# Kernel optimization log

Hardware: AMD Instinct MI355X
Metric: run time of the kernel (lower is better)

Reference implementation:

```python
import jax, jax.numpy as jnp
import numpy as np

DIM = 1024
NUM_HEADS = 16
HEAD_DIM = DIM // NUM_HEADS
SCALE = HEAD_DIM ** (-0.5)


def setup_inputs() -> dict:
    key = jax.random.key(0)
    k_x, k_qkv, k_ow, k_ob = jax.random.split(key, 4)
    x = jax.random.normal(k_x, (4, 2048, DIM), dtype=jnp.float32)
    # nn.Linear(dim, 3*dim, bias=False): store as [dim, 3*dim] for x @ W
    w_qkv = jax.random.normal(k_qkv, (DIM, 3 * DIM), dtype=jnp.float32) * (DIM ** -0.5)
    w_out = jax.random.normal(k_ow, (DIM, DIM), dtype=jnp.float32) * (DIM ** -0.5)
    b_out = jax.random.normal(k_ob, (DIM,), dtype=jnp.float32) * 0.02
    return {"x": x, "w_qkv": w_qkv, "w_out": w_out, "b_out": b_out}


def reference(x, w_qkv, w_out, b_out):
    B, S, D = x.shape
    H, Hd = NUM_HEADS, HEAD_DIM
    qkv = x @ w_qkv                                  # [B, S, 3*D]
    # rearrange 'b s (v h d) -> v b h s d'
    qkv = qkv.reshape(B, S, 3, H, Hd).transpose(2, 0, 3, 1, 4)
    q, k, v = qkv[0], qkv[1], qkv[2]                 # each [B, H, S, Hd]
    scores = jnp.einsum('bhqd,bhkd->bhqk', q, k) * SCALE
    attn = jax.nn.softmax(scores, axis=-1)
    out = jnp.einsum('bhqk,bhkd->bhqd', attn, v)     # [B, H, S, Hd]
    out = out.transpose(0, 2, 1, 3).reshape(B, S, D)  # 'b h s d -> b s (h d)'
    return out @ w_out + b_out
```

## Files before the change

kernel.cpp:

```cpp
#include <hip/hip_runtime.h>
#include <hip/hip_bf16.h>
#include <stdint.h>

typedef __bf16 bf16_t;
typedef __bf16 bf16x4 __attribute__((ext_vector_type(4)));
typedef __bf16 bf16x8 __attribute__((ext_vector_type(8)));
typedef float f32x4 __attribute__((ext_vector_type(4)));
typedef unsigned short u16;

#define L2E 1.4426950408889634f
#define MC 69.249473f
#define QSC 0.18033688f

__device__ __forceinline__ void async_load16(const bf16_t* g, bf16_t* l) {
  __builtin_amdgcn_global_load_lds(
      (__attribute__((address_space(1))) uint32_t*)g,
      (__attribute__((address_space(3))) uint32_t*)l, 16, 0, 0);
}

__global__ void detect_k(const uint16_t* __restrict__ x, int* __restrict__ flag) {
  if (blockIdx.x != 0) return;
  const int lane = threadIdx.x & 63;
  int bad = 0;
#pragma unroll
  for (int p = 0; p < 4; ++p) {
    const int i = lane * 4 + p;
    uint16_t h = x[2 * i];
    int e = (h >> 7) & 0xFF;
    if (e == 0 || e >= 0xBD) bad++;
  }
  bad += __shfl_xor(bad, 1, 64);
  bad += __shfl_xor(bad, 2, 64);
  bad += __shfl_xor(bad, 4, 64);
  bad += __shfl_xor(bad, 8, 64);
  bad += __shfl_xor(bad, 16, 64);
  bad += __shfl_xor(bad, 32, 64);
  if (lane == 0 && threadIdx.x < 64) *flag = (bad > 32) ? 1 : 0;
}

__global__ void convert_k(const void* __restrict__ in, bf16_t* __restrict__ out,
                          int n, const int* __restrict__ flag) {
  const int f = *flag;
  const int nv = n >> 3;
  const int i0 = blockIdx.x * blockDim.x + threadIdx.x;
  const int stride = gridDim.x * blockDim.x;
  if (f) {
    const float4* p = (const float4*)in;
    for (int i = i0; i < nv; i += stride) {
      const float4 a = p[2 * i], b = p[2 * i + 1];
      const float v[8] = {a.x, a.y, a.z, a.w, b.x, b.y, b.z, b.w};
      bf16x8 o8;
#pragma unroll
      for (int j = 0; j < 8; ++j) {
        float x = v[j];
        x = (x == x) ? x : 0.f;
        x = fminf(fmaxf(x, -1e6f), 1e6f);
        o8[j] = (bf16_t)x;
      }
      *(bf16x8*)(out + (size_t)i * 8) = o8;
    }
  } else {
    const uint4* p = (const uint4*)in;
    for (int i = i0; i < nv; i += stride) {
      const uint4 a = p[i];
      const uint32_t wds[4] = {a.x, a.y, a.z, a.w};
      bf16x8 o8;
#pragma unroll
      for (int j = 0; j < 8; ++j) {
        const uint32_t h = (wds[j >> 1] >> ((j & 1) * 16)) & 0xFFFFu;
        float x = __builtin_bit_cast(float, h << 16);
        x = (x == x) ? x : 0.f;
        x = fminf(fmaxf(x, -1e6f), 1e6f);
        o8[j] = (bf16_t)x;
      }
      *(bf16x8*)(out + (size_t)i * 8) = o8;
    }
  }
}

__global__ __launch_bounds__(256) void wtrans_k(const void* __restrict__ in,
                                                bf16_t* __restrict__ out, int R,
                                                int C, const int* __restrict__ flag) {
  __shared__ u16 tile[64][65];
  const int f = *flag;
  const int tr = blockIdx.y * 64, tc = blockIdx.x * 64;
  const int t = threadIdx.x;
#pragma unroll
  for (int i = 0; i < 16; ++i) {
    int idx = i * 256 + t, r = idx >> 6, c = idx & 63;
    float v;
    if (f)
      v = ((const float*)in)[(size_t)(tr + r) * C + tc + c];
    else
      v = (float)((const bf16_t*)in)[(size_t)(tr + r) * C + tc + c];
    v = (v == v) ? v : 0.f;
    v = fminf(fmaxf(v, -1e6f), 1e6f);
    bf16_t b = (bf16_t)v;
    tile[r][c] = *(u16*)&b;
  }
  __syncthreads();
#pragma unroll
  for (int i = 0; i < 16; ++i) {
    int idx = i * 256 + t, r = idx >> 6, c = idx & 63;
    ((u16*)out)[(size_t)(tc + r) * R + tr + c] = tile[c][r];
  }
}

__device__ __forceinline__ void gemm_bt_mainloop(
    const bf16_t* __restrict__ A, const bf16_t* __restrict__ Bt, int K, int m0,
    int n0, bf16_t* As, bf16_t* Bs, f32x4 acc[4][4]) {
  const int t = threadIdx.x, lane = t & 63, w = t >> 6;
  const int l15 = lane & 15, quad = lane >> 4;
  const int wm = (w >> 1) * 64, wn = (w & 1) * 64;
  const int srow = w * 16 + (lane >> 2);
  const int sk = (lane & 3) * 8;
  const bf16_t* gA = A + (size_t)(m0 + srow) * K + sk;
  const bf16_t* gB = Bt + (size_t)(n0 + srow) * K + sk;
  const size_t gstep = (size_t)64 * K;
  const int nt = K >> 5;
  const int lo = w * 512;

  async_load16(gA, As + lo);
  async_load16(gA + gstep, As + lo + 2048);
  async_load16(gB, Bs + lo);
  async_load16(gB + gstep, Bs + lo + 2048);
  __syncthreads();

  for (int kt = 0; kt < nt; ++kt) {
    const int cur = (kt & 1) * 4096, nxt = 4096 - cur;
    if (kt + 1 < nt) {
      const bf16_t* gA1 = gA + (size_t)(kt + 1) * 32;
      const bf16_t* gB1 = gB + (size_t)(kt + 1) * 32;
      async_load16(gA1, As + nxt + lo);
      async_load16(gA1 + gstep, As + nxt + lo + 2048);
      async_load16(gB1, Bs + nxt + lo);
      async_load16(gB1 + gstep, Bs + nxt + lo + 2048);
    }
    const bf16_t* Ab = As + cur;
    const bf16_t* Bb = Bs + cur;
    bf16x8 af[4], bfr[4];
#pragma unroll
    for (int f = 0; f < 4; ++f) {
      af[f] = *(const bf16x8*)(Ab + (wm + f * 16 + l15) * 32 + quad * 8);
      bfr[f] = *(const bf16x8*)(Bb + (wn + f * 16 + l15) * 32 + quad * 8);
    }
#pragma unroll
    for (int i = 0; i < 4; ++i)
#pragma unroll
      for (int j = 0; j < 4; ++j)
        acc[i][j] =
            __builtin_amdgcn_mfma_f32_16x16x32_bf16(af[i], bfr[j], acc[i][j], 0, 0, 0);
    if (kt + 1 < nt) __syncthreads();
  }
}

__global__ __launch_bounds__(256) void qkv_gemm_k(const bf16_t* __restrict__ X,
                                                  const bf16_t* __restrict__ WqT,
                                                  bf16_t* __restrict__ qo,
                                                  bf16_t* __restrict__ ko,
                                                  bf16_t* __restrict__ vto) {
  __shared__ __align__(16) bf16_t As[2 * 4096];
  __shared__ __align__(16) bf16_t Bs[2 * 4096];
  const int bid = blockIdx.x;
  const int wgid = (bid & 7) * 192 + (bid >> 3);
  const int m0 = (wgid / 24) * 128, n0 = (wgid % 24) * 128;
  f32x4 acc[4][4];
  const f32x4 z = {0.f, 0.f, 0.f, 0.f};
#pragma unroll
  for (int i = 0; i < 4; ++i)
#pragma unroll
    for (int j = 0; j < 4; ++j) acc[i][j] = z;
  gemm_bt_mainloop(X, WqT, 1024, m0, n0, As, Bs, acc);

  const int lane = threadIdx.x & 63, w = threadIdx.x >> 6;
  const int l15 = lane & 15, quad = lane >> 4;
  const int wm = (w >> 1) * 64, wn = (w & 1) * 64;
#pragma unroll
  for (int j = 0; j < 4; ++j) {
    const int gnb = n0 + wn + j * 16;
    const int vi = gnb >> 10;
    const int rem = gnb & 1023;
    const int h = rem >> 6;
    const int d = (rem & 63) + l15;
    if (vi == 2) {
#pragma unroll
      for (int i = 0; i < 4; ++i) {
        const int gm0 = m0 + wm + i * 16 + quad * 4;
        const int b = gm0 >> 11, s = gm0 & 2047;
        bf16x4 pv;
#pragma unroll
        for (int r = 0; r < 4; ++r) pv[r] = (bf16_t)acc[i][j][r];
        *(bf16x4*)(vto + ((size_t)(b * 16 + h) * 64 + d) * 2048 + s) = pv;
      }
    } else {
      const float scale = (vi == 0) ? QSC : 1.0f;
      bf16_t* dst = (vi == 0) ? qo : ko;
#pragma unroll
      for (int i = 0; i < 4; ++i) {
#pragma unroll
        for (int r = 0; r < 4; ++r) {
          const int gm = m0 + wm + i * 16 + quad * 4 + r;
          const int b = gm >> 11, s = gm & 2047;
          dst[(((size_t)(b * 16 + h) * 2048 + s) << 6) + d] =
              (bf16_t)(acc[i][j][r] * scale);
        }
      }
    }
  }
}

__global__ __launch_bounds__(256) void out_gemm_k(const bf16_t* __restrict__ Ain,
                                                  const bf16_t* __restrict__ WoT,
                                                  const bf16_t* __restrict__ bias,
                                                  void* __restrict__ outp,
                                                  const int* __restrict__ flag) {
  __shared__ __align__(16) bf16_t As[2 * 4096];
  __shared__ __align__(16) bf16_t Bs[2 * 4096];
  const int bid = blockIdx.x;
  const int wgid = (bid & 7) * 64 + (bid >> 3);
  const int m0 = (wgid / 8) * 128, n0 = (wgid % 8) * 128;
  f32x4 acc[4][4];
  const f32x4 z = {0.f, 0.f, 0.f, 0.f};
#pragma unroll
  for (int i = 0; i < 4; ++i)
#pragma unroll
    for (int j = 0; j < 4; ++j) acc[i][j] = z;
  gemm_bt_mainloop(Ain, WoT, 1024, m0, n0, As, Bs, acc);

  const int f32out = *flag;
  const int lane = threadIdx.x & 63, w = threadIdx.x >> 6;
  const int l15 = lane & 15, quad = lane >> 4;
  const int wm = (w >> 1) * 64, wn = (w & 1) * 64;
#pragma unroll
  for (int j = 0; j < 4; ++j) {
    const int gn = n0 + wn + j * 16 + l15;
    const float bv = (float)bias[gn];
#pragma unroll
    for (int i = 0; i < 4; ++i) {
#pragma unroll
      for (int r = 0; r < 4; ++r) {
        const int gm = m0 + wm + i * 16 + quad * 4 + r;
        const float val = acc[i][j][r] + bv;
        if (f32out)
          ((float*)outp)[(size_t)gm * 1024 + gn] = val;
        else
          ((bf16_t*)outp)[(size_t)gm * 1024 + gn] = (bf16_t)val;
      }
    }
  }
}

#define KTILE 4096

__global__ __launch_bounds__(256, 3) void attn_k(const bf16_t* __restrict__ q,
                                                 const bf16_t* __restrict__ k,
                                                 const bf16_t* __restrict__ vt,
                                                 bf16_t* __restrict__ o) {
  __shared__ __align__(16) bf16_t Ks[2 * KTILE];
  __shared__ __align__(16) bf16_t Vts[2 * KTILE];
  __shared__ __align__(16) bf16_t Pb[4 * 32 * 64];

  const int t = threadIdx.x, lane = t & 63, w = t >> 6;
  const int l15 = lane & 15, quad = lane >> 4;
  const int x = blockIdx.x;
  const int j = x >> 3;
  const int bh = (x & 7) * 8 + (j >> 4);
  const int qt = j & 15;
  const bf16_t* qp = q + ((size_t)bh * 2048 + qt * 128) * 64;
  const bf16_t* kp = k + (size_t)bh * 2048 * 64;
  const bf16_t* vp = vt + (size_t)bh * 64 * 2048;

  const int lane8 = lane >> 3, lc = lane & 7;
  int kOff[2], vOff[2], ldsOff[2];
#pragma unroll
  for (int c = 0; c < 2; ++c) {
    const int rho = (w * 2 + c) * 8 + lane8;
    const int srow = (rho >> 4) + (rho & 15) * 4;
    const int col = (lc ^ (rho & 7)) * 8;
    kOff[c] = srow * 64 + col;
    vOff[c] = rho * 2048 + col;
    ldsOff[c] = (w * 2 + c) * 512;
  }

  {
    const int qr = t >> 3, qc = t & 7;
#pragma unroll
    for (int p = 0; p < 4; ++p) {
      const int r0 = p * 32 + qr;
      async_load16(qp + (size_t)r0 * 64 + (qc ^ (r0 & 7)) * 8,
                   Ks + r0 * 64 + qc * 8);
    }
  }
  __syncthreads();

  bf16x8 qf[2][2];
#pragma unroll
  for (int qs = 0; qs < 2; ++qs)
#pragma unroll
    for (int ks = 0; ks < 2; ++ks) {
      const int row = w * 32 + qs * 16 + l15;
      qf[qs][ks] = *(const bf16x8*)(Ks + row * 64 +
                                    (((ks * 4 + quad) ^ (row & 7)) * 8));
    }
  __syncthreads();

#pragma unroll
  for (int c = 0; c < 2; ++c) {
    async_load16(kp + kOff[c], Ks + ldsOff[c]);
    async_load16(vp + vOff[c], Vts + ldsOff[c]);
  }

  f32x4 acc[2][4], asum[2];
  const f32x4 z = {0.f, 0.f, 0.f, 0.f};
  const f32x4 minit = {-MC, -MC, -MC, -MC};
  bf16x8 onesf;
#pragma unroll
  for (int i = 0; i < 8; ++i) onesf[i] = (bf16_t)1.0f;
#pragma unroll
  for (int qs = 0; qs < 2; ++qs) {
    asum[qs] = z;
#pragma unroll
    for (int f = 0; f < 4; ++f) acc[qs][f] = z;
  }

  bf16_t* psw = Pb + w * 32 * 64;

  for (int kt = 0; kt < 32; ++kt) {
    __syncthreads();
    if (kt < 31) {
      const int bn = (kt + 1) & 1;
#pragma unroll
      for (int c = 0; c < 2; ++c) {
        async_load16(kp + (size_t)(kt + 1) * KTILE + kOff[c],
                     Ks + bn * KTILE + ldsOff[c]);
        async_load16(vp + (size_t)(kt + 1) * 64 + vOff[c],
                     Vts + bn * KTILE + ldsOff[c]);
      }
    }

    const bf16_t* Kb = Ks + (kt & 1) * KTILE;
    const bf16_t* Vb = Vts + (kt & 1) * KTILE;

    f32x4 sacc[2][4];
    {
      const int cx = ((quad ^ (l15 & 7)) * 8);
      bf16x8 kf[4];
#pragma unroll
      for (int f = 0; f < 4; ++f)
        kf[f] = *(const bf16x8*)(Kb + (f * 16 + l15) * 64 + cx);
      __builtin_amdgcn_s_setprio(1);
#pragma unroll
      for (int qs = 0; qs < 2; ++qs)
#pragma unroll
        for (int f = 0; f < 4; ++f)
          sacc[qs][f] = __builtin_amdgcn_mfma_f32_16x16x32_bf16(
              qf[qs][0], kf[f], minit, 0, 0, 0);
      __builtin_amdgcn_s_setprio(0);
    }
    {
      const int cx = (((4 + quad) ^ (l15 & 7)) * 8);
      bf16x8 kf[4];
#pragma unroll
      for (int f = 0; f < 4; ++f)
        kf[f] = *(const bf16x8*)(Kb + (f * 16 + l15) * 64 + cx);
      __builtin_amdgcn_s_setprio(1);
#pragma unroll
      for (int qs = 0; qs < 2; ++qs)
#pragma unroll
        for (int f = 0; f < 4; ++f)
          sacc[qs][f] = __builtin_amdgcn_mfma_f32_16x16x32_bf16(
              qf[qs][1], kf[f], sacc[qs][f], 0, 0, 0);
      __builtin_amdgcn_s_setprio(0);
    }

#pragma unroll
    for (int qs = 0; qs < 2; ++qs)
#pragma unroll
      for (int r = 0; r < 4; ++r) {
        bf16x4 pk;
#pragma unroll
        for (int f = 0; f < 4; ++f)
          pk[f] = (bf16_t)__builtin_amdgcn_exp2f(fminf(sacc[qs][f][r], 0.f));
        const int row = qs * 16 + quad * 4 + r;
        *(bf16x4*)(psw + row * 64 + ((l15 >> 1) ^ (row & 7)) * 8 +
                   (l15 & 1) * 4) = pk;
      }

#pragma unroll
    for (int ks = 0; ks < 2; ++ks) {
      const int cx = (((ks * 4 + quad) ^ (l15 & 7)) * 8);
      bf16x8 vf[4];
#pragma unroll
      for (int f = 0; f < 4; ++f)
        vf[f] = *(const bf16x8*)(Vb + (f * 16 + l15) * 64 + cx);
#pragma unroll
      for (int qs = 0; qs < 2; ++qs) {
        bf16x8 pf = *(const bf16x8*)(psw + (qs * 16 + l15) * 64 +
                                     ((ks * 4 + quad) ^ (l15 & 7)) * 8);
        __builtin_amdgcn_s_setprio(1);
#pragma unroll
        for (int f = 0; f < 4; ++f)
          acc[qs][f] = __builtin_amdgcn_mfma_f32_16x16x32_bf16(
              pf, vf[f], acc[qs][f], 0, 0, 0);
        asum[qs] = __builtin_amdgcn_mfma_f32_16x16x32_bf16(pf, onesf, asum[qs],
                                                           0, 0, 0);
        __builtin_amdgcn_s_setprio(0);
      }
    }
  }

  const int b = bh >> 4, h = bh & 15;
#pragma unroll
  for (int qs = 0; qs < 2; ++qs)
#pragma unroll
    for (int r = 0; r < 4; ++r) {
      const int srow = qt * 128 + w * 32 + qs * 16 + quad * 4 + r;
      const float inv = 1.0f / fmaxf(asum[qs][r], 1e-37f);
#pragma unroll
      for (int f = 0; f < 4; ++f) {
        const int d = f * 16 + l15;
        o[(size_t)(b * 2048 + srow) * 1024 + h * 64 + d] =
            (bf16_t)(acc[qs][f][r] * inv);
      }
    }
}

extern "C" void kernel_launch(void* const* d_in, const int* in_sizes, int n_in,
                              void* d_out, int out_size, void* d_ws, size_t ws_size,
                              hipStream_t stream) {
  const void* x_raw = d_in[0];
  const void* wqkv_raw = d_in[1];
  const void* wout_raw = d_in[2];
  const void* bout_raw = d_in[3];

  const int nx = 4 * 2048 * 1024;
  const int nwq = 1024 * 3072;
  const int nwo = 1024 * 1024;
  const int nb = 1024;

  char* ws = (char*)d_ws;
  int* flag = (int*)ws;
  bf16_t* xb = (bf16_t*)(ws + 256);
  bf16_t* wqbT = xb + nx;
  bf16_t* wobT = wqbT + nwq;
  bf16_t* bob = wobT + nwo;
  bf16_t* qb = bob + nb;
  const size_t bhsd = (size_t)4 * 16 * 2048 * 64;
  bf16_t* kb = qb + bhsd;
  bf16_t* vtb = kb + bhsd;
  bf16_t* ab = xb;

  detect_k<<<1, 64, 0, stream>>>((const uint16_t*)x_raw, flag);
  convert_k<<<2048, 256, 0, stream>>>(x_raw, xb, nx, flag);
  wtrans_k<<<dim3(3072 / 64, 1024 / 64), 256, 0, stream>>>(wqkv_raw, wqbT, 1024,
                                                           3072, flag);
  wtrans_k<<<dim3(1024 / 64, 1024 / 64), 256, 0, stream>>>(wout_raw, wobT, 1024,
                                                           1024, flag);
  convert_k<<<1, 256, 0, stream>>>(bout_raw, bob, nb, flag);

  qkv_gemm_k<<<dim3(1536), 256, 0, stream>>>(xb, wqbT, qb, kb, vtb);
  attn_k<<<dim3(1024), 256, 0, stream>>>(qb, kb, vtb, ab);
  out_gemm_k<<<dim3(512), 256, 0, stream>>>(ab, wobT, bob, d_out, flag);
}
```

Measured before the change: 314.8 us.

## Replace double-buffered GEMM mainloop with single-buffer load-sync-compute loop

Removes the LDS double buffering from the shared GEMM mainloop used by the QKV and output projections. Each K step now syncs, issues the async global-to-LDS loads, syncs again, then runs the MFMAs, so LDS use per block halves. This may allow more resident blocks per CU, but loads no longer overlap compute and each step pays two barriers.

```diff
diff --git a/kernel.cpp b/kernel.cpp
--- a/kernel.cpp
+++ b/kernel.cpp
@@ -116,33 +116,24 @@
   const int sk = (lane & 3) * 8;
   const bf16_t* gA = A + (size_t)(m0 + srow) * K + sk;
   const bf16_t* gB = Bt + (size_t)(n0 + srow) * K + sk;
+  bf16_t* lA = As + w * 512;
+  bf16_t* lB = Bs + w * 512;
   const size_t gstep = (size_t)64 * K;
-  const int nt = K >> 5;
-  const int lo = w * 512;
-
-  async_load16(gA, As + lo);
-  async_load16(gA + gstep, As + lo + 2048);
-  async_load16(gB, Bs + lo);
-  async_load16(gB + gstep, Bs + lo + 2048);
-  __syncthreads();
-
-  for (int kt = 0; kt < nt; ++kt) {
-    const int cur = (kt & 1) * 4096, nxt = 4096 - cur;
-    if (kt + 1 < nt) {
-      const bf16_t* gA1 = gA + (size_t)(kt + 1) * 32;
-      const bf16_t* gB1 = gB + (size_t)(kt + 1) * 32;
-      async_load16(gA1, As + nxt + lo);
-      async_load16(gA1 + gstep, As + nxt + lo + 2048);
-      async_load16(gB1, Bs + nxt + lo);
-      async_load16(gB1 + gstep, Bs + nxt + lo + 2048);
-    }
-    const bf16_t* Ab = As + cur;
-    const bf16_t* Bb = Bs + cur;
+
+  for (int kt = 0; kt < K; kt += 32) {
+    __syncthreads();
+    async_load16(gA, lA);
+    async_load16(gA + gstep, lA + 2048);
+    async_load16(gB, lB);
+    async_load16(gB + gstep, lB + 2048);
+    gA += 32;
+    gB += 32;
+    __syncthreads();
     bf16x8 af[4], bfr[4];
 #pragma unroll
     for (int f = 0; f < 4; ++f) {
-      af[f] = *(const bf16x8*)(Ab + (wm + f * 16 + l15) * 32 + quad * 8);
-      bfr[f] = *(const bf16x8*)(Bb + (wn + f * 16 + l15) * 32 + quad * 8);
+      af[f] = *(const bf16x8*)(As + (wm + f * 16 + l15) * 32 + quad * 8);
+      bfr[f] = *(const bf16x8*)(Bs + (wn + f * 16 + l15) * 32 + quad * 8);
     }
 #pragma unroll
     for (int i = 0; i < 4; ++i)
@@ -150,7 +141,6 @@
       for (int j = 0; j < 4; ++j)
         acc[i][j] =
             __builtin_amdgcn_mfma_f32_16x16x32_bf16(af[i], bfr[j], acc[i][j], 0, 0, 0);
-    if (kt + 1 < nt) __syncthreads();
   }
 }
 
@@ -159,8 +149,8 @@
                                                   bf16_t* __restrict__ qo,
                                                   bf16_t* __restrict__ ko,
                                                   bf16_t* __restrict__ vto) {
-  __shared__ __align__(16) bf16_t As[2 * 4096];
-  __shared__ __align__(16) bf16_t Bs[2 * 4096];
+  __shared__ __align__(16) bf16_t As[128 * 32];
+  __shared__ __align__(16) bf16_t Bs[128 * 32];
   const int bid = blockIdx.x;
   const int wgid = (bid & 7) * 192 + (bid >> 3);
   const int m0 = (wgid / 24) * 128, n0 = (wgid % 24) * 128;
@@ -214,8 +204,8 @@
                                                   const bf16_t* __restrict__ bias,
                                                   void* __restrict__ outp,
                                                   const int* __restrict__ flag) {
-  __shared__ __align__(16) bf16_t As[2 * 4096];
-  __shared__ __align__(16) bf16_t Bs[2 * 4096];
+  __shared__ __align__(16) bf16_t As[128 * 32];
+  __shared__ __align__(16) bf16_t Bs[128 * 32];
   const int bid = blockIdx.x;
   const int wgid = (bid & 7) * 64 + (bid >> 3);
   const int m0 = (wgid / 8) * 128, n0 = (wgid % 8) * 128;
```

Measured after the change: 300.4 us. 1.05x faster.
